# Performance work log

Measured on AMD Instinct MI355X. Metric: run time of the kernel, lower is better.

The kernel has to match this reference:

```python
import jax, jax.numpy as jnp
import numpy as np
import math

DIM = 1024
HEADS = 16
DIM_HEAD = 64
INNER = HEADS * DIM_HEAD
NUM_BUCKETS = 32
MAX_DISTANCE = 128


def setup_inputs() -> dict:
    key = jax.random.key(0)
    ks = jax.random.split(key, 6)
    x = jax.random.normal(ks[0], (2, 2048, DIM), dtype=jnp.float32)
    Wq = jax.random.normal(ks[1], (DIM, INNER), dtype=jnp.float32) * (DIM ** -0.5)
    Wkv = jax.random.normal(ks[2], (DIM, 2 * DIM_HEAD), dtype=jnp.float32) * (DIM ** -0.5)
    Wout = jax.random.normal(ks[3], (INNER, DIM), dtype=jnp.float32) * (INNER ** -0.5)
    bout = jnp.zeros((DIM,), dtype=jnp.float32)
    rel_emb = jax.random.normal(ks[4], (NUM_BUCKETS, HEADS), dtype=jnp.float32) * 0.02
    return {"x": x, "Wq": Wq, "Wkv": Wkv, "Wout": Wout, "bout": bout, "rel_emb": rel_emb}


def _relative_position_bucket(rel_pos, num_buckets=NUM_BUCKETS, max_distance=MAX_DISTANCE):
    # rel_pos: [i, j] int32, k_pos - q_pos
    n = jnp.maximum(-rel_pos, 0)
    max_exact = num_buckets // 2
    is_small = n < max_exact
    n_safe = jnp.maximum(n, 1)  # avoid log(0); masked by is_small anyway
    val_if_large = max_exact + (
        jnp.log(n_safe.astype(jnp.float32) / max_exact)
        / math.log(max_distance / max_exact)
        * (num_buckets - max_exact)
    ).astype(jnp.int32)
    val_if_large = jnp.minimum(val_if_large, num_buckets - 1)
    return jnp.where(is_small, n, val_if_large)


def reference(x, Wq, Wkv, Wout, bout, rel_emb):
    b, n, _ = x.shape
    scale = DIM_HEAD ** -0.5
    bias_scale = DIM_HEAD ** 0.5

    q = (x @ Wq).reshape(b, n, HEADS, DIM_HEAD).transpose(0, 2, 1, 3) * scale  # [b,h,n,d]
    kv = x @ Wkv  # [b,n,2d]
    k, v = kv[..., :DIM_HEAD], kv[..., DIM_HEAD:]  # shared single-head K/V [b,n,d]

    sim = jnp.einsum('bhid,bjd->bhij', q, k)

    # T5 relative position bias
    pos = jnp.arange(n, dtype=jnp.int32)
    rel_pos = pos[None, :] - pos[:, None]  # [i,j] = k_pos - q_pos
    rp_bucket = _relative_position_bucket(rel_pos)
    bias = rel_emb[rp_bucket]  # [i,j,h]
    sim = sim + jnp.transpose(bias, (2, 0, 1))[None] * bias_scale

    # causal mask: mask strictly-upper triangle
    causal_mask = jnp.triu(jnp.ones((n, n), dtype=bool), k=1)
    neg = jnp.finfo(sim.dtype).max
    sim = jnp.where(causal_mask[None, None], -neg, sim)

    attn = jax.nn.softmax(sim, axis=-1)
    out = jnp.einsum('bhij,bjd->bhid', attn, v)
    out = out.transpose(0, 2, 1, 3).reshape(b, n, INNER)
    return out @ Wout + bout
```

## Files before the change

kernel.cpp:

```cpp
#include <hip/hip_runtime.h>
#include <cstdint>
#include <cmath>

typedef _Float16 half8 __attribute__((ext_vector_type(8)));
typedef unsigned short ushort8 __attribute__((ext_vector_type(8)));
typedef float floatx4 __attribute__((ext_vector_type(4)));

#define VT_STRIDE 2080

__device__ __forceinline__ unsigned short f2h(float f) {
    union { _Float16 h; unsigned short u; } cv;
    cv.h = (_Float16)f;
    return cv.u;
}

__device__ __forceinline__ void gld_lds16(const unsigned short* g, unsigned short* l) {
    __builtin_amdgcn_global_load_lds(
        (const __attribute__((address_space(1))) unsigned int*)g,
        (__attribute__((address_space(3))) unsigned int*)l, 16, 0, 0);
}

__global__ void cast_x_kernel(const float* __restrict__ x, unsigned short* __restrict__ xh, int n8) {
    int idx = blockIdx.x * blockDim.x + threadIdx.x;
    if (idx >= n8) return;
    const float4* p = (const float4*)x;
    float4 a = p[idx * 2], b = p[idx * 2 + 1];
    ushort8 o;
    o[0] = f2h(a.x); o[1] = f2h(a.y); o[2] = f2h(a.z); o[3] = f2h(a.w);
    o[4] = f2h(b.x); o[5] = f2h(b.y); o[6] = f2h(b.z); o[7] = f2h(b.w);
    *(ushort8*)(xh + (size_t)idx * 8) = o;
}

__global__ void transpose_fused_kernel(const float* __restrict__ Wq, const float* __restrict__ Wkv,
                                       const float* __restrict__ Wout,
                                       unsigned short* __restrict__ Wqkvt, unsigned short* __restrict__ Wot) {
    __shared__ float tile[32][33];
    int bxi = blockIdx.x;
    const float* in; unsigned short* out; int C; int cb;
    if (bxi < 32)      { in = Wq;   out = Wqkvt;                 C = 1024; cb = bxi; }
    else if (bxi < 36) { in = Wkv;  out = Wqkvt + 1024 * 1024;   C = 128;  cb = bxi - 32; }
    else               { in = Wout; out = Wot;                   C = 1024; cb = bxi - 36; }
    int bx = cb * 32, by = blockIdx.y * 32;
    int x = threadIdx.x, y0 = threadIdx.y;
    #pragma unroll
    for (int k = 0; k < 4; k++) {
        int y = y0 + k * 8;
        tile[y][x] = in[(size_t)(by + y) * C + bx + x];
    }
    __syncthreads();
    #pragma unroll
    for (int k = 0; k < 4; k++) {
        int y = y0 + k * 8;
        out[(size_t)(bx + y) * 1024 + by + x] = f2h(tile[x][y]);
    }
}

template<int MODE>
__global__ __launch_bounds__(256) void gemm_mn(
    const unsigned short* __restrict__ A, const unsigned short* __restrict__ Bt,
    unsigned short* __restrict__ oq, unsigned short* __restrict__ ok,
    unsigned short* __restrict__ ov, float* __restrict__ of,
    const float* __restrict__ bias)
{
    __shared__ __align__(16) unsigned short As[2][64 * 64];
    __shared__ __align__(16) unsigned short Bs[2][128 * 64];
    const int K = 1024;
    int t = threadIdx.x;
    int w = t >> 6, lane = t & 63, g = lane >> 4, il = lane & 15;
    int wr = w >> 1, wc = w & 1;
    int m0 = blockIdx.x * 64, n0 = blockIdx.y * 128;

    int l8 = lane >> 3, b8 = lane & 7;
    int swz = (b8 ^ l8) * 8;
    const unsigned short* Ag = A  + (size_t)(m0 + w * 16 + l8) * K + swz;
    const unsigned short* Bg = Bt + (size_t)(n0 + w * 32 + l8) * K + swz;
    int e0 = (g ^ (il & 7)) * 8;

    floatx4 acc[2][4] = {};

    #pragma unroll
    for (int q = 0; q < 2; q++)
        gld_lds16(Ag + (size_t)(q * 8) * K, &As[0][(w * 16 + q * 8) * 64]);
    #pragma unroll
    for (int q = 0; q < 4; q++)
        gld_lds16(Bg + (size_t)(q * 8) * K, &Bs[0][(w * 32 + q * 8) * 64]);

    int cb = 0;
    for (int k0 = 0; k0 < K; k0 += 64, cb ^= 1) {
        if (k0 + 64 < K) {
            #pragma unroll
            for (int q = 0; q < 2; q++)
                gld_lds16(Ag + (size_t)(q * 8) * K + k0 + 64, &As[cb ^ 1][(w * 16 + q * 8) * 64]);
            #pragma unroll
            for (int q = 0; q < 4; q++)
                gld_lds16(Bg + (size_t)(q * 8) * K + k0 + 64, &Bs[cb ^ 1][(w * 32 + q * 8) * 64]);
            asm volatile("s_waitcnt vmcnt(6)" ::: "memory");
        } else {
            asm volatile("s_waitcnt vmcnt(0)" ::: "memory");
        }
        __builtin_amdgcn_s_barrier();
        __builtin_amdgcn_sched_barrier(0);

        const unsigned short* Ac = &As[cb][0];
        const unsigned short* Bc = &Bs[cb][0];
        #pragma unroll
        for (int ks = 0; ks < 2; ks++) {
            half8 a[2];
            #pragma unroll
            for (int mt = 0; mt < 2; mt++)
                a[mt] = *(const half8*)&Ac[(wr * 32 + mt * 16 + il) * 64 + (e0 ^ (ks * 32))];
            #pragma unroll
            for (int nt = 0; nt < 4; nt++) {
                half8 b = *(const half8*)&Bc[(wc * 64 + nt * 16 + il) * 64 + (e0 ^ (ks * 32))];
                #pragma unroll
                for (int mt = 0; mt < 2; mt++)
                    acc[mt][nt] = __builtin_amdgcn_mfma_f32_16x16x32_f16(a[mt], b, acc[mt][nt], 0, 0, 0);
            }
        }
        asm volatile("s_waitcnt lgkmcnt(0)" ::: "memory");
        __builtin_amdgcn_s_barrier();
    }

    #pragma unroll
    for (int mt = 0; mt < 2; mt++) {
        #pragma unroll
        for (int nt = 0; nt < 4; nt++) {
            #pragma unroll
            for (int r = 0; r < 4; r++) {
                int row = m0 + wr * 32 + mt * 16 + 4 * g + r;
                int col = n0 + wc * 64 + nt * 16 + il;
                float v = acc[mt][nt][r];
                if (MODE == 0) {
                    if (col < 1024) {
                        int b = row >> 11, i = row & 2047, h = col >> 6, d = col & 63;
                        oq[(size_t)((b * 16 + h) * 2048 + i) * 64 + d] = f2h(v * 0.18033688011112042f);
                    } else if (col < 1088) {
                        ok[(size_t)row * 64 + (col - 1024)] = f2h(v);
                    } else {
                        int b = row >> 11, j = row & 2047;
                        ov[(size_t)((b << 6) + (col - 1088)) * VT_STRIDE + j] = f2h(v);
                    }
                } else {
                    of[(size_t)row * 1024 + col] = v + bias[col];
                }
            }
        }
    }
}

__global__ __launch_bounds__(256) void attn_kernel(
    const unsigned short* __restrict__ qh, const unsigned short* __restrict__ kh,
    const unsigned short* __restrict__ vt, const float* __restrict__ rel_emb,
    unsigned short* __restrict__ ob)
{
    __shared__ float bias_tab[256];
    __shared__ __align__(16) unsigned short Ks[2][64 * 64];
    __shared__ __align__(16) unsigned short Vs[64 * 64];
    __shared__ __align__(16) unsigned short Pl[64 * 72];

    int bx = 31 - blockIdx.y;
    int bh = blockIdx.x;
    int b = bh >> 4, h = bh & 15;
    int t = threadIdx.x;
    int w = t >> 6, lane = t & 63, g = lane >> 4, il = lane & 15;

    float cbv = rel_emb[31 * 16 + h];
    {
        int dlt = t;
        int bucket;
        if (dlt < 16) bucket = dlt;
        else {
            float lg = logf((float)dlt * 0.0625f) / 2.0794415416798357f;
            int vv = 16 + (int)(lg * 16.0f);
            bucket = vv < 31 ? vv : 31;
        }
        bias_tab[dlt] = (rel_emb[bucket * 16 + h] - cbv) * 11.541560327111708f;
    }

    const unsigned short* kbase = kh + (size_t)b * (2048 * 64);
    const unsigned short* vbase = vt + (size_t)b * (64 * VT_STRIDE);
    int prow = (w * 16 + il) * 72;

    int l8 = lane >> 3, b8 = lane & 7;
    int swz = (b8 ^ l8) * 8;
    const unsigned short* kg_base = kbase + (size_t)(w * 16 + l8) * 64 + swz;
    const unsigned short* vg_base = vbase + (size_t)(w * 16 + l8) * VT_STRIDE + swz;
    int e0 = (g ^ (il & 7)) * 8;

    int iw = bx * 64 + w * 16;
    int i_glob = iw + il;
    const unsigned short* qrow = qh + (size_t)(bh * 2048 + i_glob) * 64;
    half8 qf0 = *(const half8*)(qrow + g * 8);
    half8 qf1 = *(const half8*)(qrow + 32 + g * 8);
    floatx4 O[4] = {};
    float m_run = -1e30f, l_run = 0.0f;

    gld_lds16(kg_base,                 &Ks[0][(w * 16) * 64]);
    gld_lds16(kg_base + 8 * 64,        &Ks[0][(w * 16 + 8) * 64]);
    gld_lds16(vg_base,                 &Vs[(w * 16) * 64]);
    gld_lds16(vg_base + 8 * VT_STRIDE, &Vs[(w * 16 + 8) * 64]);

    for (int c = 0; c <= bx; c++) {
        __syncthreads();
        if (c < bx) {
            const unsigned short* kg = kg_base + (size_t)(c + 1) * 4096;
            unsigned short* kd = &Ks[(c + 1) & 1][0];
            gld_lds16(kg,          &kd[(w * 16) * 64]);
            gld_lds16(kg + 8 * 64, &kd[(w * 16 + 8) * 64]);
        }
        const unsigned short* Kc = &Ks[c & 1][0];
        int j0 = c * 64;

        floatx4 S[4] = {};
        #pragma unroll
        for (int jt = 0; jt < 4; jt++) {
            half8 k0 = *(const half8*)&Kc[jt * 1024 + il * 64 + e0];
            half8 k1 = *(const half8*)&Kc[jt * 1024 + il * 64 + (e0 ^ 32)];
            S[jt] = __builtin_amdgcn_mfma_f32_16x16x32_f16(k0, qf0, S[jt], 0, 0, 0);
            S[jt] = __builtin_amdgcn_mfma_f32_16x16x32_f16(k1, qf1, S[jt], 0, 0, 0);
        }
        half8 vf[8];
        #pragma unroll
        for (int ks = 0; ks < 2; ks++)
            #pragma unroll
            for (int dt = 0; dt < 4; dt++)
                vf[ks * 4 + dt] = *(const half8*)&Vs[dt * 1024 + il * 64 + (e0 ^ (ks * 32))];

        asm volatile("s_waitcnt lgkmcnt(0)" ::: "memory");
        __builtin_amdgcn_s_barrier();
        if (c < bx) {
            const unsigned short* vg = vg_base + (c + 1) * 64;
            gld_lds16(vg,                 &Vs[(w * 16) * 64]);
            gld_lds16(vg + 8 * VT_STRIDE, &Vs[(w * 16 + 8) * 64]);
        }

        float s[16];
        if (c + 3 <= bx) {
            #pragma unroll
            for (int q2 = 0; q2 < 16; q2++) s[q2] = S[q2 >> 2][q2 & 3];
        } else if (c < bx) {
            #pragma unroll
            for (int jt = 0; jt < 4; jt++)
                #pragma unroll
                for (int r = 0; r < 4; r++)
                    s[jt * 4 + r] = S[jt][r] + bias_tab[i_glob - (j0 + jt * 16 + 4 * g + r)];
        } else {
            #pragma unroll
            for (int jt = 0; jt < 4; jt++) {
                #pragma unroll
                for (int r = 0; r < 4; r++) {
                    int delta = i_glob - (j0 + jt * 16 + 4 * g + r);
                    int di = delta > 0 ? delta : 0;
                    s[jt * 4 + r] = (delta >= 0) ? (S[jt][r] + bias_tab[di]) : -1e30f;
                }
            }
        }
        float m8[8];
        #pragma unroll
        for (int q2 = 0; q2 < 8; q2++) m8[q2] = fmaxf(s[q2], s[q2 + 8]);
        #pragma unroll
        for (int q2 = 0; q2 < 4; q2++) m8[q2] = fmaxf(m8[q2], m8[q2 + 4]);
        float mx = fmaxf(fmaxf(m8[0], m8[1]), fmaxf(m8[2], m8[3]));
        mx = fmaxf(mx, __shfl_xor(mx, 16));
        mx = fmaxf(mx, __shfl_xor(mx, 32));
        if (__any(mx > m_run)) {
            float m_new = fmaxf(m_run, mx);
            float alpha = __builtin_amdgcn_exp2f(m_run - m_new);
            l_run *= alpha;
            float arow[4];
            #pragma unroll
            for (int r = 0; r < 4; r++) arow[r] = __shfl(alpha, 4 * g + r);
            #pragma unroll
            for (int dt = 0; dt < 4; dt++)
                #pragma unroll
                for (int r = 0; r < 4; r++) O[dt][r] *= arow[r];
            m_run = m_new;
        }
        float p[16];
        #pragma unroll
        for (int q2 = 0; q2 < 16; q2++) p[q2] = __builtin_amdgcn_exp2f(s[q2] - m_run);
        float ps[8];
        #pragma unroll
        for (int q2 = 0; q2 < 8; q2++) ps[q2] = p[q2] + p[q2 + 8];
        #pragma unroll
        for (int q2 = 0; q2 < 4; q2++) ps[q2] += ps[q2 + 4];
        float psum = (ps[0] + ps[1]) + (ps[2] + ps[3]);
        psum += __shfl_xor(psum, 16);
        psum += __shfl_xor(psum, 32);
        l_run += psum;

        #pragma unroll
        for (int jt = 0; jt < 4; jt++) {
            uint2 u;
            u.x = (unsigned int)f2h(p[jt * 4 + 0]) | ((unsigned int)f2h(p[jt * 4 + 1]) << 16);
            u.y = (unsigned int)f2h(p[jt * 4 + 2]) | ((unsigned int)f2h(p[jt * 4 + 3]) << 16);
            *(uint2*)&Pl[prow + jt * 16 + 4 * g] = u;
        }
        #pragma unroll
        for (int ks = 0; ks < 2; ks++) {
            half8 pf = *(const half8*)&Pl[prow + ks * 32 + g * 8];
            #pragma unroll
            for (int dt = 0; dt < 4; dt++)
                O[dt] = __builtin_amdgcn_mfma_f32_16x16x32_f16(pf, vf[ks * 4 + dt], O[dt], 0, 0, 0);
        }
    }
    float inv[4];
    #pragma unroll
    for (int r = 0; r < 4; r++) inv[r] = 1.0f / __shfl(l_run, 4 * g + r);
    #pragma unroll
    for (int dt = 0; dt < 4; dt++) {
        #pragma unroll
        for (int r = 0; r < 4; r++) {
            int i = iw + 4 * g + r;
            int d = dt * 16 + il;
            ob[(size_t)(b * 2048 + i) * 1024 + h * 64 + d] = f2h(O[dt][r] * inv[r]);
        }
    }
}

extern "C" void kernel_launch(void* const* d_in, const int* in_sizes, int n_in,
                              void* d_out, int out_size, void* d_ws, size_t ws_size,
                              hipStream_t stream) {
    const float* x    = (const float*)d_in[0];
    const float* Wq   = (const float*)d_in[1];
    const float* Wkv  = (const float*)d_in[2];
    const float* Wout = (const float*)d_in[3];
    const float* bout = (const float*)d_in[4];
    const float* rel  = (const float*)d_in[5];
    float* out = (float*)d_out;

    unsigned short* ws    = (unsigned short*)d_ws;
    unsigned short* xh    = ws;
    unsigned short* qh    = xh + 4194304;
    unsigned short* kh    = qh + 4194304;
    unsigned short* vt    = kh + 262144;
    unsigned short* Wqkvt = vt + 2 * 64 * VT_STRIDE;
    unsigned short* Wot   = Wqkvt + 1179648;
    unsigned short* ob    = xh;

    cast_x_kernel<<<2048, 256, 0, stream>>>(x, xh, 524288);
    transpose_fused_kernel<<<dim3(68, 32), dim3(32, 8), 0, stream>>>(Wq, Wkv, Wout, Wqkvt, Wot);
    gemm_mn<0><<<dim3(64, 9), 256, 0, stream>>>(xh, Wqkvt, qh, kh, vt, nullptr, nullptr);
    attn_kernel<<<dim3(32, 32), 256, 0, stream>>>(qh, kh, vt, rel, ob);
    gemm_mn<2><<<dim3(64, 8), 256, 0, stream>>>(ob, Wot, nullptr, nullptr, nullptr, out, bout);
}
```

Measured before the change: 167.1 us.

## Single-buffer B tile with register prefetch; unconditional online-softmax rescale

The GEMM now keeps a single LDS buffer for the B tile. It loads A/B fragments into registers, then issues the next B global-to-LDS load after a barrier, overlapping it with the MFMAs. This cuts LDS use, which may allow more blocks per CU, but adds a barrier per iteration and removes the vmcnt wait that guarded the previous loads. In attention, the far-field bias is folded in as an absolute offset rather than subtracted from the table, and the softmax rescale is applied every tile instead of behind a wave-wide branch, trading divergence for extra multiplies.

```diff
diff --git a/kernel.cpp b/kernel.cpp
--- a/kernel.cpp
+++ b/kernel.cpp
@@ -63,7 +63,7 @@
     const float* __restrict__ bias)
 {
     __shared__ __align__(16) unsigned short As[2][64 * 64];
-    __shared__ __align__(16) unsigned short Bs[2][128 * 64];
+    __shared__ __align__(16) unsigned short Bs[128 * 64];
     const int K = 1024;
     int t = threadIdx.x;
     int w = t >> 6, lane = t & 63, g = lane >> 4, il = lane & 15;
@@ -83,42 +83,40 @@
         gld_lds16(Ag + (size_t)(q * 8) * K, &As[0][(w * 16 + q * 8) * 64]);
     #pragma unroll
     for (int q = 0; q < 4; q++)
-        gld_lds16(Bg + (size_t)(q * 8) * K, &Bs[0][(w * 32 + q * 8) * 64]);
+        gld_lds16(Bg + (size_t)(q * 8) * K, &Bs[(w * 32 + q * 8) * 64]);
 
     int cb = 0;
     for (int k0 = 0; k0 < K; k0 += 64, cb ^= 1) {
+        __syncthreads();
         if (k0 + 64 < K) {
             #pragma unroll
             for (int q = 0; q < 2; q++)
                 gld_lds16(Ag + (size_t)(q * 8) * K + k0 + 64, &As[cb ^ 1][(w * 16 + q * 8) * 64]);
+        }
+        half8 af[2][2], bf[2][4];
+        #pragma unroll
+        for (int ks = 0; ks < 2; ks++) {
+            #pragma unroll
+            for (int mt = 0; mt < 2; mt++)
+                af[ks][mt] = *(const half8*)&As[cb][(wr * 32 + mt * 16 + il) * 64 + (e0 ^ (ks * 32))];
+            #pragma unroll
+            for (int nt = 0; nt < 4; nt++)
+                bf[ks][nt] = *(const half8*)&Bs[(wc * 64 + nt * 16 + il) * 64 + (e0 ^ (ks * 32))];
+        }
+        asm volatile("s_waitcnt lgkmcnt(0)" ::: "memory");
+        __builtin_amdgcn_s_barrier();
+        if (k0 + 64 < K) {
             #pragma unroll
             for (int q = 0; q < 4; q++)
-                gld_lds16(Bg + (size_t)(q * 8) * K + k0 + 64, &Bs[cb ^ 1][(w * 32 + q * 8) * 64]);
-            asm volatile("s_waitcnt vmcnt(6)" ::: "memory");
-        } else {
-            asm volatile("s_waitcnt vmcnt(0)" ::: "memory");
-        }
-        __builtin_amdgcn_s_barrier();
-        __builtin_amdgcn_sched_barrier(0);
-
-        const unsigned short* Ac = &As[cb][0];
-        const unsigned short* Bc = &Bs[cb][0];
-        #pragma unroll
-        for (int ks = 0; ks < 2; ks++) {
-            half8 a[2];
-            #pragma unroll
-            for (int mt = 0; mt < 2; mt++)
-                a[mt] = *(const half8*)&Ac[(wr * 32 + mt * 16 + il) * 64 + (e0 ^ (ks * 32))];
-            #pragma unroll
-            for (int nt = 0; nt < 4; nt++) {
-                half8 b = *(const half8*)&Bc[(wc * 64 + nt * 16 + il) * 64 + (e0 ^ (ks * 32))];
+                gld_lds16(Bg + (size_t)(q * 8) * K + k0 + 64, &Bs[(w * 32 + q * 8) * 64]);
+        }
+        #pragma unroll
+        for (int ks = 0; ks < 2; ks++)
+            #pragma unroll
+            for (int nt = 0; nt < 4; nt++)
                 #pragma unroll
                 for (int mt = 0; mt < 2; mt++)
-                    acc[mt][nt] = __builtin_amdgcn_mfma_f32_16x16x32_f16(a[mt], b, acc[mt][nt], 0, 0, 0);
-            }
-        }
-        asm volatile("s_waitcnt lgkmcnt(0)" ::: "memory");
-        __builtin_amdgcn_s_barrier();
+                    acc[mt][nt] = __builtin_amdgcn_mfma_f32_16x16x32_f16(af[ks][mt], bf[ks][nt], acc[mt][nt], 0, 0, 0);
     }
 
     #pragma unroll
@@ -164,7 +162,6 @@
     int t = threadIdx.x;
     int w = t >> 6, lane = t & 63, g = lane >> 4, il = lane & 15;
 
-    float cbv = rel_emb[31 * 16 + h];
     {
         int dlt = t;
         int bucket;
@@ -174,8 +171,9 @@
             int vv = 16 + (int)(lg * 16.0f);
             bucket = vv < 31 ? vv : 31;
         }
-        bias_tab[dlt] = (rel_emb[bucket * 16 + h] - cbv) * 11.541560327111708f;
-    }
+        bias_tab[dlt] = rel_emb[bucket * 16 + h] * 11.541560327111708f;
+    }
+    float cb31 = rel_emb[31 * 16 + h] * 11.541560327111708f;
 
     const unsigned short* kbase = kh + (size_t)b * (2048 * 64);
     const unsigned short* vbase = vt + (size_t)b * (64 * VT_STRIDE);
@@ -237,7 +235,7 @@
         float s[16];
         if (c + 3 <= bx) {
             #pragma unroll
-            for (int q2 = 0; q2 < 16; q2++) s[q2] = S[q2 >> 2][q2 & 3];
+            for (int q2 = 0; q2 < 16; q2++) s[q2] = S[q2 >> 2][q2 & 3] + cb31;
         } else if (c < bx) {
             #pragma unroll
             for (int jt = 0; jt < 4; jt++)
@@ -263,22 +261,11 @@
         float mx = fmaxf(fmaxf(m8[0], m8[1]), fmaxf(m8[2], m8[3]));
         mx = fmaxf(mx, __shfl_xor(mx, 16));
         mx = fmaxf(mx, __shfl_xor(mx, 32));
-        if (__any(mx > m_run)) {
-            float m_new = fmaxf(m_run, mx);
-            float alpha = __builtin_amdgcn_exp2f(m_run - m_new);
-            l_run *= alpha;
-            float arow[4];
-            #pragma unroll
-            for (int r = 0; r < 4; r++) arow[r] = __shfl(alpha, 4 * g + r);
-            #pragma unroll
-            for (int dt = 0; dt < 4; dt++)
-                #pragma unroll
-                for (int r = 0; r < 4; r++) O[dt][r] *= arow[r];
-            m_run = m_new;
-        }
+        float m_new = fmaxf(m_run, mx);
+        float alpha = __builtin_amdgcn_exp2f(m_run - m_new);
         float p[16];
         #pragma unroll
-        for (int q2 = 0; q2 < 16; q2++) p[q2] = __builtin_amdgcn_exp2f(s[q2] - m_run);
+        for (int q2 = 0; q2 < 16; q2++) p[q2] = __builtin_amdgcn_exp2f(s[q2] - m_new);
         float ps[8];
         #pragma unroll
         for (int q2 = 0; q2 < 8; q2++) ps[q2] = p[q2] + p[q2 + 8];
@@ -287,7 +274,15 @@
         float psum = (ps[0] + ps[1]) + (ps[2] + ps[3]);
         psum += __shfl_xor(psum, 16);
         psum += __shfl_xor(psum, 32);
-        l_run += psum;
+        l_run = l_run * alpha + psum;
+        m_run = m_new;
+        float arow[4];
+        #pragma unroll
+        for (int r = 0; r < 4; r++) arow[r] = __shfl(alpha, 4 * g + r);
+        #pragma unroll
+        for (int dt = 0; dt < 4; dt++)
+            #pragma unroll
+            for (int r = 0; r < 4; r++) O[dt][r] *= arow[r];
 
         #pragma unroll
         for (int jt = 0; jt < 4; jt++) {
```

New measurement: 170.7 us. +2.2%, slower.

## Process two query tiles per attention block and merge cast/transpose prep kernels

Applied to the files above, without the earlier changes.

Each attention workgroup now handles two adjacent 64-row query tiles (128 rows), so every K/V chunk loaded into LDS is reused by both tiles, halving K/V traffic and barrier count per query row. The grid shrinks to 16 row-blocks per head, and the online softmax drops its conditional rescale in favour of an unconditional update. The x cast and the weight transposes are merged into one prep launch to save a kernel launch. The trade-off is more registers per thread and fewer workgroups, which could reduce occupancy or leave the grid load-imbalanced.

```diff
diff --git a/kernel.cpp b/kernel.cpp
--- a/kernel.cpp
+++ b/kernel.cpp
@@ -20,38 +20,41 @@
         (__attribute__((address_space(3))) unsigned int*)l, 16, 0, 0);
 }
 
-__global__ void cast_x_kernel(const float* __restrict__ x, unsigned short* __restrict__ xh, int n8) {
-    int idx = blockIdx.x * blockDim.x + threadIdx.x;
-    if (idx >= n8) return;
-    const float4* p = (const float4*)x;
-    float4 a = p[idx * 2], b = p[idx * 2 + 1];
-    ushort8 o;
-    o[0] = f2h(a.x); o[1] = f2h(a.y); o[2] = f2h(a.z); o[3] = f2h(a.w);
-    o[4] = f2h(b.x); o[5] = f2h(b.y); o[6] = f2h(b.z); o[7] = f2h(b.w);
-    *(ushort8*)(xh + (size_t)idx * 8) = o;
-}
-
-__global__ void transpose_fused_kernel(const float* __restrict__ Wq, const float* __restrict__ Wkv,
-                                       const float* __restrict__ Wout,
-                                       unsigned short* __restrict__ Wqkvt, unsigned short* __restrict__ Wot) {
+__global__ void prep_kernel(const float* __restrict__ x,
+                            const float* __restrict__ Wq, const float* __restrict__ Wkv,
+                            const float* __restrict__ Wout,
+                            unsigned short* __restrict__ xh,
+                            unsigned short* __restrict__ Wqkvt, unsigned short* __restrict__ Wot) {
+    int bxi = blockIdx.x;
+    if (bxi >= 68) {
+        int fb = (bxi - 68) * 32 + blockIdx.y;
+        int tt = threadIdx.y * 32 + threadIdx.x;
+        int idx = fb * 256 + tt;
+        const float4* p = (const float4*)x;
+        float4 a = p[idx * 2], b = p[idx * 2 + 1];
+        ushort8 o;
+        o[0] = f2h(a.x); o[1] = f2h(a.y); o[2] = f2h(a.z); o[3] = f2h(a.w);
+        o[4] = f2h(b.x); o[5] = f2h(b.y); o[6] = f2h(b.z); o[7] = f2h(b.w);
+        *(ushort8*)(xh + (size_t)idx * 8) = o;
+        return;
+    }
     __shared__ float tile[32][33];
-    int bxi = blockIdx.x;
     const float* in; unsigned short* out; int C; int cb;
     if (bxi < 32)      { in = Wq;   out = Wqkvt;                 C = 1024; cb = bxi; }
     else if (bxi < 36) { in = Wkv;  out = Wqkvt + 1024 * 1024;   C = 128;  cb = bxi - 32; }
     else               { in = Wout; out = Wot;                   C = 1024; cb = bxi - 36; }
     int bx = cb * 32, by = blockIdx.y * 32;
-    int x = threadIdx.x, y0 = threadIdx.y;
+    int xx = threadIdx.x, y0 = threadIdx.y;
     #pragma unroll
     for (int k = 0; k < 4; k++) {
         int y = y0 + k * 8;
-        tile[y][x] = in[(size_t)(by + y) * C + bx + x];
+        tile[y][xx] = in[(size_t)(by + y) * C + bx + xx];
     }
     __syncthreads();
     #pragma unroll
     for (int k = 0; k < 4; k++) {
         int y = y0 + k * 8;
-        out[(size_t)(bx + y) * 1024 + by + x] = f2h(tile[x][y]);
+        out[(size_t)(bx + y) * 1024 + by + xx] = f2h(tile[xx][y]);
     }
 }
 
@@ -156,15 +159,14 @@
     __shared__ float bias_tab[256];
     __shared__ __align__(16) unsigned short Ks[2][64 * 64];
     __shared__ __align__(16) unsigned short Vs[64 * 64];
-    __shared__ __align__(16) unsigned short Pl[64 * 72];
-
-    int bx = 31 - blockIdx.y;
+    __shared__ __align__(16) unsigned short Pl[128 * 72];
+
+    int r = 15 - blockIdx.y;
     int bh = blockIdx.x;
     int b = bh >> 4, h = bh & 15;
     int t = threadIdx.x;
     int w = t >> 6, lane = t & 63, g = lane >> 4, il = lane & 15;
 
-    float cbv = rel_emb[31 * 16 + h];
     {
         int dlt = t;
         int bucket;
@@ -174,12 +176,14 @@
             int vv = 16 + (int)(lg * 16.0f);
             bucket = vv < 31 ? vv : 31;
         }
-        bias_tab[dlt] = (rel_emb[bucket * 16 + h] - cbv) * 11.541560327111708f;
-    }
+        bias_tab[dlt] = rel_emb[bucket * 16 + h] * 11.541560327111708f;
+    }
+    float cb31 = rel_emb[31 * 16 + h] * 11.541560327111708f;
 
     const unsigned short* kbase = kh + (size_t)b * (2048 * 64);
     const unsigned short* vbase = vt + (size_t)b * (64 * VT_STRIDE);
-    int prow = (w * 16 + il) * 72;
+    int prowA = (w * 16 + il) * 72;
+    int prowB = (64 + w * 16 + il) * 72;
 
     int l8 = lane >> 3, b8 = lane & 7;
     int swz = (b8 ^ l8) * 8;
@@ -187,22 +191,27 @@
     const unsigned short* vg_base = vbase + (size_t)(w * 16 + l8) * VT_STRIDE + swz;
     int e0 = (g ^ (il & 7)) * 8;
 
-    int iw = bx * 64 + w * 16;
-    int i_glob = iw + il;
-    const unsigned short* qrow = qh + (size_t)(bh * 2048 + i_glob) * 64;
-    half8 qf0 = *(const half8*)(qrow + g * 8);
-    half8 qf1 = *(const half8*)(qrow + 32 + g * 8);
-    floatx4 O[4] = {};
-    float m_run = -1e30f, l_run = 0.0f;
+    int bxA = 2 * r, bxB = 2 * r + 1;
+    int iwA = r * 128 + w * 16;
+    int iwB = iwA + 64;
+    int iA = iwA + il, iB = iwB + il;
+    const unsigned short* qrowA = qh + (size_t)(bh * 2048 + iA) * 64;
+    const unsigned short* qrowB = qh + (size_t)(bh * 2048 + iB) * 64;
+    half8 qA0 = *(const half8*)(qrowA + g * 8);
+    half8 qA1 = *(const half8*)(qrowA + 32 + g * 8);
+    half8 qB0 = *(const half8*)(qrowB + g * 8);
+    half8 qB1 = *(const half8*)(qrowB + 32 + g * 8);
+    floatx4 OA[4] = {}, OB[4] = {};
+    float mA = -1e30f, lA = 0.0f, mB = -1e30f, lB = 0.0f;
 
     gld_lds16(kg_base,                 &Ks[0][(w * 16) * 64]);
     gld_lds16(kg_base + 8 * 64,        &Ks[0][(w * 16 + 8) * 64]);
     gld_lds16(vg_base,                 &Vs[(w * 16) * 64]);
     gld_lds16(vg_base + 8 * VT_STRIDE, &Vs[(w * 16 + 8) * 64]);
 
-    for (int c = 0; c <= bx; c++) {
+    for (int c = 0; c <= bxB; c++) {
         __syncthreads();
-        if (c < bx) {
+        if (c < bxB) {
             const unsigned short* kg = kg_base + (size_t)(c + 1) * 4096;
             unsigned short* kd = &Ks[(c + 1) & 1][0];
             gld_lds16(kg,          &kd[(w * 16) * 64]);
@@ -210,14 +219,19 @@
         }
         const unsigned short* Kc = &Ks[c & 1][0];
         int j0 = c * 64;
-
-        floatx4 S[4] = {};
+        bool doA = (c <= bxA);
+
+        floatx4 SA[4] = {}, SB[4] = {};
         #pragma unroll
         for (int jt = 0; jt < 4; jt++) {
             half8 k0 = *(const half8*)&Kc[jt * 1024 + il * 64 + e0];
             half8 k1 = *(const half8*)&Kc[jt * 1024 + il * 64 + (e0 ^ 32)];
-            S[jt] = __builtin_amdgcn_mfma_f32_16x16x32_f16(k0, qf0, S[jt], 0, 0, 0);
-            S[jt] = __builtin_amdgcn_mfma_f32_16x16x32_f16(k1, qf1, S[jt], 0, 0, 0);
+            if (doA) {
+                SA[jt] = __builtin_amdgcn_mfma_f32_16x16x32_f16(k0, qA0, SA[jt], 0, 0, 0);
+                SA[jt] = __builtin_amdgcn_mfma_f32_16x16x32_f16(k1, qA1, SA[jt], 0, 0, 0);
+            }
+            SB[jt] = __builtin_amdgcn_mfma_f32_16x16x32_f16(k0, qB0, SB[jt], 0, 0, 0);
+            SB[jt] = __builtin_amdgcn_mfma_f32_16x16x32_f16(k1, qB1, SB[jt], 0, 0, 0);
         }
         half8 vf[8];
         #pragma unroll
@@ -228,92 +242,159 @@
 
         asm volatile("s_waitcnt lgkmcnt(0)" ::: "memory");
         __builtin_amdgcn_s_barrier();
-        if (c < bx) {
+        if (c < bxB) {
             const unsigned short* vg = vg_base + (c + 1) * 64;
             gld_lds16(vg,                 &Vs[(w * 16) * 64]);
             gld_lds16(vg + 8 * VT_STRIDE, &Vs[(w * 16 + 8) * 64]);
         }
 
-        float s[16];
-        if (c + 3 <= bx) {
-            #pragma unroll
-            for (int q2 = 0; q2 < 16; q2++) s[q2] = S[q2 >> 2][q2 & 3];
-        } else if (c < bx) {
-            #pragma unroll
-            for (int jt = 0; jt < 4; jt++)
-                #pragma unroll
-                for (int r = 0; r < 4; r++)
-                    s[jt * 4 + r] = S[jt][r] + bias_tab[i_glob - (j0 + jt * 16 + 4 * g + r)];
-        } else {
+        if (doA) {
+            float s[16];
+            if (c + 3 <= bxA) {
+                #pragma unroll
+                for (int q2 = 0; q2 < 16; q2++) s[q2] = SA[q2 >> 2][q2 & 3] + cb31;
+            } else if (c < bxA) {
+                #pragma unroll
+                for (int jt = 0; jt < 4; jt++)
+                    #pragma unroll
+                    for (int r4 = 0; r4 < 4; r4++)
+                        s[jt * 4 + r4] = SA[jt][r4] + bias_tab[iA - (j0 + jt * 16 + 4 * g + r4)];
+            } else {
+                #pragma unroll
+                for (int jt = 0; jt < 4; jt++) {
+                    #pragma unroll
+                    for (int r4 = 0; r4 < 4; r4++) {
+                        int delta = iA - (j0 + jt * 16 + 4 * g + r4);
+                        int di = delta > 0 ? delta : 0;
+                        s[jt * 4 + r4] = (delta >= 0) ? (SA[jt][r4] + bias_tab[di]) : -1e30f;
+                    }
+                }
+            }
+            float m8[8];
+            #pragma unroll
+            for (int q2 = 0; q2 < 8; q2++) m8[q2] = fmaxf(s[q2], s[q2 + 8]);
+            #pragma unroll
+            for (int q2 = 0; q2 < 4; q2++) m8[q2] = fmaxf(m8[q2], m8[q2 + 4]);
+            float mx = fmaxf(fmaxf(m8[0], m8[1]), fmaxf(m8[2], m8[3]));
+            mx = fmaxf(mx, __shfl_xor(mx, 16));
+            mx = fmaxf(mx, __shfl_xor(mx, 32));
+            float m_new = fmaxf(mA, mx);
+            float alpha = __builtin_amdgcn_exp2f(mA - m_new);
+            #pragma unroll
+            for (int q2 = 0; q2 < 16; q2++) s[q2] = __builtin_amdgcn_exp2f(s[q2] - m_new);
+            float ps[8];
+            #pragma unroll
+            for (int q2 = 0; q2 < 8; q2++) ps[q2] = s[q2] + s[q2 + 8];
+            #pragma unroll
+            for (int q2 = 0; q2 < 4; q2++) ps[q2] += ps[q2 + 4];
+            float psum = (ps[0] + ps[1]) + (ps[2] + ps[3]);
+            psum += __shfl_xor(psum, 16);
+            psum += __shfl_xor(psum, 32);
+            lA = lA * alpha + psum;
+            mA = m_new;
+            float arow[4];
+            #pragma unroll
+            for (int r4 = 0; r4 < 4; r4++) arow[r4] = __shfl(alpha, 4 * g + r4);
+            #pragma unroll
+            for (int dt = 0; dt < 4; dt++)
+                #pragma unroll
+                for (int r4 = 0; r4 < 4; r4++) OA[dt][r4] *= arow[r4];
             #pragma unroll
             for (int jt = 0; jt < 4; jt++) {
-                #pragma unroll
-                for (int r = 0; r < 4; r++) {
-                    int delta = i_glob - (j0 + jt * 16 + 4 * g + r);
-                    int di = delta > 0 ? delta : 0;
-                    s[jt * 4 + r] = (delta >= 0) ? (S[jt][r] + bias_tab[di]) : -1e30f;
+                uint2 u;
+                u.x = (unsigned int)f2h(s[jt * 4 + 0]) | ((unsigned int)f2h(s[jt * 4 + 1]) << 16);
+                u.y = (unsigned int)f2h(s[jt * 4 + 2]) | ((unsigned int)f2h(s[jt * 4 + 3]) << 16);
+                *(uint2*)&Pl[prowA + jt * 16 + 4 * g] = u;
+            }
+        }
+        {
+            float s[16];
+            if (c + 3 <= bxB) {
+                #pragma unroll
+                for (int q2 = 0; q2 < 16; q2++) s[q2] = SB[q2 >> 2][q2 & 3] + cb31;
+            } else if (c < bxB) {
+                #pragma unroll
+                for (int jt = 0; jt < 4; jt++)
+                    #pragma unroll
+                    for (int r4 = 0; r4 < 4; r4++)
+                        s[jt * 4 + r4] = SB[jt][r4] + bias_tab[iB - (j0 + jt * 16 + 4 * g + r4)];
+            } else {
+                #pragma unroll
+                for (int jt = 0; jt < 4; jt++) {
+                    #pragma unroll
+                    for (int r4 = 0; r4 < 4; r4++) {
+                        int delta = iB - (j0 + jt * 16 + 4 * g + r4);
+                        int di = delta > 0 ? delta : 0;
+                        s[jt * 4 + r4] = (delta >= 0) ? (SB[jt][r4] + bias_tab[di]) : -1e30f;
+                    }
                 }
             }
-        }
-        float m8[8];
-        #pragma unroll
-        for (int q2 = 0; q2 < 8; q2++) m8[q2] = fmaxf(s[q2], s[q2 + 8]);
-        #pragma unroll
-        for (int q2 = 0; q2 < 4; q2++) m8[q2] = fmaxf(m8[q2], m8[q2 + 4]);
-        float mx = fmaxf(fmaxf(m8[0], m8[1]), fmaxf(m8[2], m8[3]));
-        mx = fmaxf(mx, __shfl_xor(mx, 16));
-        mx = fmaxf(mx, __shfl_xor(mx, 32));
-        if (__any(mx > m_run)) {
-            float m_new = fmaxf(m_run, mx);
-            float alpha = __builtin_amdgcn_exp2f(m_run - m_new);
-            l_run *= alpha;
+            float m8[8];
+            #pragma unroll
+            for (int q2 = 0; q2 < 8; q2++) m8[q2] = fmaxf(s[q2], s[q2 + 8]);
+            #pragma unroll
+            for (int q2 = 0; q2 < 4; q2++) m8[q2] = fmaxf(m8[q2], m8[q2 + 4]);
+            float mx = fmaxf(fmaxf(m8[0], m8[1]), fmaxf(m8[2], m8[3]));
+            mx = fmaxf(mx, __shfl_xor(mx, 16));
+            mx = fmaxf(mx, __shfl_xor(mx, 32));
+            float m_new = fmaxf(mB, mx);
+            float alpha = __builtin_amdgcn_exp2f(mB - m_new);
+            #pragma unroll
+            for (int q2 = 0; q2 < 16; q2++) s[q2] = __builtin_amdgcn_exp2f(s[q2] - m_new);
+            float ps[8];
+            #pragma unroll
+            for (int q2 = 0; q2 < 8; q2++) ps[q2] = s[q2] + s[q2 + 8];
+            #pragma unroll
+            for (int q2 = 0; q2 < 4; q2++) ps[q2] += ps[q2 + 4];
+            float psum = (ps[0] + ps[1]) + (ps[2] + ps[3]);
+            psum += __shfl_xor(psum, 16);
+            psum += __shfl_xor(psum, 32);
+            lB = lB * alpha + psum;
+            mB = m_new;
             float arow[4];
             #pragma unroll
-            for (int r = 0; r < 4; r++) arow[r] = __shfl(alpha, 4 * g + r);
+            for (int r4 = 0; r4 < 4; r4++) arow[r4] = __shfl(alpha, 4 * g + r4);
             #pragma unroll
             for (int dt = 0; dt < 4; dt++)
                 #pragma unroll
-                for (int r = 0; r < 4; r++) O[dt][r] *= arow[r];
-            m_run = m_new;
-        }
-        float p[16];
-        #pragma unroll
-        for (int q2 = 0; q2 < 16; q2++) p[q2] = __builtin_amdgcn_exp2f(s[q2] - m_run);
-        float ps[8];
-        #pragma unroll
-        for (int q2 = 0; q2 < 8; q2++) ps[q2] = p[q2] + p[q2 + 8];
-        #pragma unroll
-        for (int q2 = 0; q2 < 4; q2++) ps[q2] += ps[q2 + 4];
-        float psum = (ps[0] + ps[1]) + (ps[2] + ps[3]);
-        psum += __shfl_xor(psum, 16);
-        psum += __shfl_xor(psum, 32);
-        l_run += psum;
-
-        #pragma unroll
-        for (int jt = 0; jt < 4; jt++) {
-            uint2 u;
-            u.x = (unsigned int)f2h(p[jt * 4 + 0]) | ((unsigned int)f2h(p[jt * 4 + 1]) << 16);
-            u.y = (unsigned int)f2h(p[jt * 4 + 2]) | ((unsigned int)f2h(p[jt * 4 + 3]) << 16);
-            *(uint2*)&Pl[prow + jt * 16 + 4 * g] = u;
+                for (int r4 = 0; r4 < 4; r4++) OB[dt][r4] *= arow[r4];
+            #pragma unroll
+            for (int jt = 0; jt < 4; jt++) {
+                uint2 u;
+                u.x = (unsigned int)f2h(s[jt * 4 + 0]) | ((unsigned int)f2h(s[jt * 4 + 1]) << 16);
+                u.y = (unsigned int)f2h(s[jt * 4 + 2]) | ((unsigned int)f2h(s[jt * 4 + 3]) << 16);
+                *(uint2*)&Pl[prowB + jt * 16 + 4 * g] = u;
+            }
         }
         #pragma unroll
         for (int ks = 0; ks < 2; ks++) {
-            half8 pf = *(const half8*)&Pl[prow + ks * 32 + g * 8];
+            half8 pfB = *(const half8*)&Pl[prowB + ks * 32 + g * 8];
             #pragma unroll
             for (int dt = 0; dt < 4; dt++)
-                O[dt] = __builtin_amdgcn_mfma_f32_16x16x32_f16(pf, vf[ks * 4 + dt], O[dt], 0, 0, 0);
-        }
-    }
-    float inv[4];
-    #pragma unroll
-    for (int r = 0; r < 4; r++) inv[r] = 1.0f / __shfl(l_run, 4 * g + r);
+                OB[dt] = __builtin_amdgcn_mfma_f32_16x16x32_f16(pfB, vf[ks * 4 + dt], OB[dt], 0, 0, 0);
+        }
+        if (doA) {
+            #pragma unroll
+            for (int ks = 0; ks < 2; ks++) {
+                half8 pfA = *(const half8*)&Pl[prowA + ks * 32 + g * 8];
+                #pragma unroll
+                for (int dt = 0; dt < 4; dt++)
+                    OA[dt] = __builtin_amdgcn_mfma_f32_16x16x32_f16(pfA, vf[ks * 4 + dt], OA[dt], 0, 0, 0);
+            }
+        }
+    }
+    float invA[4], invB[4];
+    #pragma unroll
+    for (int r4 = 0; r4 < 4; r4++) invA[r4] = 1.0f / __shfl(lA, 4 * g + r4);
+    #pragma unroll
+    for (int r4 = 0; r4 < 4; r4++) invB[r4] = 1.0f / __shfl(lB, 4 * g + r4);
     #pragma unroll
     for (int dt = 0; dt < 4; dt++) {
         #pragma unroll
-        for (int r = 0; r < 4; r++) {
-            int i = iw + 4 * g + r;
+        for (int r4 = 0; r4 < 4; r4++) {
             int d = dt * 16 + il;
-            ob[(size_t)(b * 2048 + i) * 1024 + h * 64 + d] = f2h(O[dt][r] * inv[r]);
+            ob[(size_t)(b * 2048 + iwA + 4 * g + r4) * 1024 + h * 64 + d] = f2h(OA[dt][r4] * invA[r4]);
+            ob[(size_t)(b * 2048 + iwB + 4 * g + r4) * 1024 + h * 64 + d] = f2h(OB[dt][r4] * invB[r4]);
         }
     }
 }
@@ -338,9 +419,8 @@
     unsigned short* Wot   = Wqkvt + 1179648;
     unsigned short* ob    = xh;
 
-    cast_x_kernel<<<2048, 256, 0, stream>>>(x, xh, 524288);
-    transpose_fused_kernel<<<dim3(68, 32), dim3(32, 8), 0, stream>>>(Wq, Wkv, Wout, Wqkvt, Wot);
+    prep_kernel<<<dim3(132, 32), dim3(32, 8), 0, stream>>>(x, Wq, Wkv, Wout, xh, Wqkvt, Wot);
     gemm_mn<0><<<dim3(64, 9), 256, 0, stream>>>(xh, Wqkvt, qh, kh, vt, nullptr, nullptr);
-    attn_kernel<<<dim3(32, 32), 256, 0, stream>>>(qh, kh, vt, rel, ob);
+    attn_kernel<<<dim3(32, 16), 256, 0, stream>>>(qh, kh, vt, rel, ob);
     gemm_mn<2><<<dim3(64, 8), 256, 0, stream>>>(ob, Wot, nullptr, nullptr, nullptr, out, bout);
 }
```

New measurement: 185.4 us. +10.9%, slower.

## Merge x cast into weight-transpose kernel and make softmax rescale unconditional

Applied to the files above, without the earlier changes.

Folds the fp32-to-fp16 cast of x into the weight transpose launch as extra blocks, removing one kernel launch. In attention, the bias table now stores absolute scaled rel_emb values, and the far-distance constant bias is added explicitly to the fully-unmasked tiles instead of being subtracted from the table. The online-softmax rescale is made branch-free: alpha is computed and O is rescaled every tile instead of only when a wave sees a new max. This removes the divergent __any vote at the cost of extra multiplies per tile.

```diff
diff --git a/kernel.cpp b/kernel.cpp
--- a/kernel.cpp
+++ b/kernel.cpp
@@ -20,38 +20,41 @@
         (__attribute__((address_space(3))) unsigned int*)l, 16, 0, 0);
 }
 
-__global__ void cast_x_kernel(const float* __restrict__ x, unsigned short* __restrict__ xh, int n8) {
-    int idx = blockIdx.x * blockDim.x + threadIdx.x;
-    if (idx >= n8) return;
-    const float4* p = (const float4*)x;
-    float4 a = p[idx * 2], b = p[idx * 2 + 1];
-    ushort8 o;
-    o[0] = f2h(a.x); o[1] = f2h(a.y); o[2] = f2h(a.z); o[3] = f2h(a.w);
-    o[4] = f2h(b.x); o[5] = f2h(b.y); o[6] = f2h(b.z); o[7] = f2h(b.w);
-    *(ushort8*)(xh + (size_t)idx * 8) = o;
-}
-
-__global__ void transpose_fused_kernel(const float* __restrict__ Wq, const float* __restrict__ Wkv,
-                                       const float* __restrict__ Wout,
-                                       unsigned short* __restrict__ Wqkvt, unsigned short* __restrict__ Wot) {
+__global__ void prep_kernel(const float* __restrict__ x,
+                            const float* __restrict__ Wq, const float* __restrict__ Wkv,
+                            const float* __restrict__ Wout,
+                            unsigned short* __restrict__ xh,
+                            unsigned short* __restrict__ Wqkvt, unsigned short* __restrict__ Wot) {
+    int bxi = blockIdx.x;
+    if (bxi >= 68) {
+        int fb = (bxi - 68) * 32 + blockIdx.y;
+        int tt = threadIdx.y * 32 + threadIdx.x;
+        int idx = fb * 256 + tt;
+        const float4* p = (const float4*)x;
+        float4 a = p[idx * 2], b = p[idx * 2 + 1];
+        ushort8 o;
+        o[0] = f2h(a.x); o[1] = f2h(a.y); o[2] = f2h(a.z); o[3] = f2h(a.w);
+        o[4] = f2h(b.x); o[5] = f2h(b.y); o[6] = f2h(b.z); o[7] = f2h(b.w);
+        *(ushort8*)(xh + (size_t)idx * 8) = o;
+        return;
+    }
     __shared__ float tile[32][33];
-    int bxi = blockIdx.x;
     const float* in; unsigned short* out; int C; int cb;
     if (bxi < 32)      { in = Wq;   out = Wqkvt;                 C = 1024; cb = bxi; }
     else if (bxi < 36) { in = Wkv;  out = Wqkvt + 1024 * 1024;   C = 128;  cb = bxi - 32; }
     else               { in = Wout; out = Wot;                   C = 1024; cb = bxi - 36; }
     int bx = cb * 32, by = blockIdx.y * 32;
-    int x = threadIdx.x, y0 = threadIdx.y;
+    int xx = threadIdx.x, y0 = threadIdx.y;
     #pragma unroll
     for (int k = 0; k < 4; k++) {
         int y = y0 + k * 8;
-        tile[y][x] = in[(size_t)(by + y) * C + bx + x];
+        tile[y][xx] = in[(size_t)(by + y) * C + bx + xx];
     }
     __syncthreads();
     #pragma unroll
     for (int k = 0; k < 4; k++) {
         int y = y0 + k * 8;
-        out[(size_t)(bx + y) * 1024 + by + x] = f2h(tile[x][y]);
+        out[(size_t)(bx + y) * 1024 + by + xx] = f2h(tile[xx][y]);
     }
 }
 
@@ -164,7 +167,6 @@
     int t = threadIdx.x;
     int w = t >> 6, lane = t & 63, g = lane >> 4, il = lane & 15;
 
-    float cbv = rel_emb[31 * 16 + h];
     {
         int dlt = t;
         int bucket;
@@ -174,8 +176,9 @@
             int vv = 16 + (int)(lg * 16.0f);
             bucket = vv < 31 ? vv : 31;
         }
-        bias_tab[dlt] = (rel_emb[bucket * 16 + h] - cbv) * 11.541560327111708f;
-    }
+        bias_tab[dlt] = rel_emb[bucket * 16 + h] * 11.541560327111708f;
+    }
+    float cb31 = rel_emb[31 * 16 + h] * 11.541560327111708f;
 
     const unsigned short* kbase = kh + (size_t)b * (2048 * 64);
     const unsigned short* vbase = vt + (size_t)b * (64 * VT_STRIDE);
@@ -237,7 +240,7 @@
         float s[16];
         if (c + 3 <= bx) {
             #pragma unroll
-            for (int q2 = 0; q2 < 16; q2++) s[q2] = S[q2 >> 2][q2 & 3];
+            for (int q2 = 0; q2 < 16; q2++) s[q2] = S[q2 >> 2][q2 & 3] + cb31;
         } else if (c < bx) {
             #pragma unroll
             for (int jt = 0; jt < 4; jt++)
@@ -263,22 +266,11 @@
         float mx = fmaxf(fmaxf(m8[0], m8[1]), fmaxf(m8[2], m8[3]));
         mx = fmaxf(mx, __shfl_xor(mx, 16));
         mx = fmaxf(mx, __shfl_xor(mx, 32));
-        if (__any(mx > m_run)) {
-            float m_new = fmaxf(m_run, mx);
-            float alpha = __builtin_amdgcn_exp2f(m_run - m_new);
-            l_run *= alpha;
-            float arow[4];
-            #pragma unroll
-            for (int r = 0; r < 4; r++) arow[r] = __shfl(alpha, 4 * g + r);
-            #pragma unroll
-            for (int dt = 0; dt < 4; dt++)
-                #pragma unroll
-                for (int r = 0; r < 4; r++) O[dt][r] *= arow[r];
-            m_run = m_new;
-        }
+        float m_new = fmaxf(m_run, mx);
+        float alpha = __builtin_amdgcn_exp2f(m_run - m_new);
         float p[16];
         #pragma unroll
-        for (int q2 = 0; q2 < 16; q2++) p[q2] = __builtin_amdgcn_exp2f(s[q2] - m_run);
+        for (int q2 = 0; q2 < 16; q2++) p[q2] = __builtin_amdgcn_exp2f(s[q2] - m_new);
         float ps[8];
         #pragma unroll
         for (int q2 = 0; q2 < 8; q2++) ps[q2] = p[q2] + p[q2 + 8];
@@ -287,7 +279,15 @@
         float psum = (ps[0] + ps[1]) + (ps[2] + ps[3]);
         psum += __shfl_xor(psum, 16);
         psum += __shfl_xor(psum, 32);
-        l_run += psum;
+        l_run = l_run * alpha + psum;
+        m_run = m_new;
+        float arow[4];
+        #pragma unroll
+        for (int r = 0; r < 4; r++) arow[r] = __shfl(alpha, 4 * g + r);
+        #pragma unroll
+        for (int dt = 0; dt < 4; dt++)
+            #pragma unroll
+            for (int r = 0; r < 4; r++) O[dt][r] *= arow[r];
 
         #pragma unroll
         for (int jt = 0; jt < 4; jt++) {
@@ -338,8 +338,7 @@
     unsigned short* Wot   = Wqkvt + 1179648;
     unsigned short* ob    = xh;
 
-    cast_x_kernel<<<2048, 256, 0, stream>>>(x, xh, 524288);
-    transpose_fused_kernel<<<dim3(68, 32), dim3(32, 8), 0, stream>>>(Wq, Wkv, Wout, Wqkvt, Wot);
+    prep_kernel<<<dim3(132, 32), dim3(32, 8), 0, stream>>>(x, Wq, Wkv, Wout, xh, Wqkvt, Wot);
     gemm_mn<0><<<dim3(64, 9), 256, 0, stream>>>(xh, Wqkvt, qh, kh, vt, nullptr, nullptr);
     attn_kernel<<<dim3(32, 32), 256, 0, stream>>>(qh, kh, vt, rel, ob);
     gemm_mn<2><<<dim3(64, 8), 256, 0, stream>>>(ob, Wot, nullptr, nullptr, nullptr, out, bout);
```

New measurement: 159.2 us. 1.05x faster.
